# Optimization experiments

Hardware: AMD Instinct MI355X
Metric: run time of the kernel (lower is better)

Reference implementation:

```python
import jax, jax.numpy as jnp
import numpy as np

N, T, H, D = 32, 2048, 1024, 384

def setup_inputs() -> dict:
    key = jax.random.key(0)
    k1, k2, k3, k4, k5 = jax.random.split(key, 5)
    scale_h = 1.0 / np.sqrt(H)
    scale_d = 1.0 / np.sqrt(D)
    return {
        "gru_output": jax.random.normal(k1, (N, T, H), dtype=jnp.float32),
        "condition": jax.random.normal(k2, (N, D), dtype=jnp.float32),
        "W_h": jax.random.normal(k3, (H, H), dtype=jnp.float32) * scale_h,
        "W_c": jax.random.normal(k4, (D, H), dtype=jnp.float32) * scale_d,
        "bias": jnp.zeros((H,), dtype=jnp.float32),
        "v": jax.random.normal(k5, (H,), dtype=jnp.float32) * scale_h,
    }

def reference(gru_output, condition, W_h, W_c, bias, v):
    # h_proj: (N, T, H); c_proj: (N, 1, H)
    h_proj = jnp.einsum("nth,hk->ntk", gru_output, W_h)
    c_proj = jnp.einsum("nd,dk->nk", condition, W_c)[:, None, :]
    energy = jnp.tanh(h_proj + c_proj + bias)          # (N, T, H)
    scores = jnp.einsum("ntk,k->nt", energy, v)        # (N, T)
    weights = jax.nn.softmax(scores, axis=-1)          # (N, T)
    context = jnp.einsum("nth,nt->nh", gru_output, weights)  # (N, H)
    return context
```

## Files before the change

### kernel.cpp

```cpp
#include <hip/hip_runtime.h>
#include <hip/hip_bf16.h>

#define N_B 32
#define T_S 2048
#define H_D 1024
#define D_C 384
#define NT  (N_B * T_S)

typedef __attribute__((ext_vector_type(8))) short bf16x8;
typedef __attribute__((ext_vector_type(4))) float f32x4;

__device__ __forceinline__ ushort f2bf(float f) {
    union { float f; unsigned u; } x; x.f = f;
    unsigned u = x.u;
    unsigned r = (u + 0x7FFFu + ((u >> 16) & 1u)) >> 16;
    return (ushort)r;
}

__device__ __forceinline__ float bf2f(ushort u) {
    union { unsigned u; float f; } x; x.u = ((unsigned)u) << 16;
    return x.f;
}

__device__ __forceinline__ float fast_tanh(float x) {
    float e = __expf(2.0f * x);
    return 1.0f - 2.0f / (e + 1.0f);
}

__device__ __forceinline__ void gl2lds16(const void* g, void* l) {
    __builtin_amdgcn_global_load_lds(
        (const __attribute__((address_space(1))) void*)g,
        (__attribute__((address_space(3))) void*)l, 16, 0, 0);
}

__global__ __launch_bounds__(256) void convert_kernel(
    const float* __restrict__ g, ushort* __restrict__ gb)
{
    const size_t base = ((size_t)blockIdx.x * 256 + threadIdx.x) * 4;
    float4 v = *(const float4*)(g + base);
    ushort4 o;
    o.x = f2bf(v.x); o.y = f2bf(v.y); o.z = f2bf(v.z); o.w = f2bf(v.w);
    *(ushort4*)(gb + base) = o;
}

__global__ __launch_bounds__(256) void transpose_kernel(
    const float* __restrict__ W, ushort* __restrict__ Wt)
{
    __shared__ ushort tile[64 * 66];
    const int bx = blockIdx.x & 15;
    const int by = blockIdx.x >> 4;
    const int t = threadIdx.x;
    #pragma unroll
    for (int i = 0; i < 16; ++i) {
        int idx = t + i * 256;
        int r = idx >> 6, c = idx & 63;
        tile[r * 66 + c] = f2bf(W[(size_t)(by * 64 + r) * H_D + bx * 64 + c]);
    }
    __syncthreads();
    #pragma unroll
    for (int i = 0; i < 16; ++i) {
        int idx = t + i * 256;
        int r = idx >> 6, c = idx & 63;
        Wt[(size_t)(bx * 64 + r) * H_D + by * 64 + c] = tile[c * 66 + r];
    }
}

__global__ __launch_bounds__(256) void cproj_kernel(
    const float* __restrict__ cond, const float* __restrict__ Wc,
    const float* __restrict__ bias, float* __restrict__ cproj)
{
    const int idx = blockIdx.x * 256 + threadIdx.x;
    const int n = idx >> 10, k = idx & 1023;
    const int d0 = blockIdx.y * 96;
    float a0 = (blockIdx.y == 0) ? bias[k] : 0.f;
    float a1 = 0.f, a2 = 0.f, a3 = 0.f;
    const float* cp = cond + n * D_C;
    for (int d = d0; d < d0 + 96; d += 4) {
        a0 = fmaf(cp[d + 0], Wc[(size_t)(d + 0) * H_D + k], a0);
        a1 = fmaf(cp[d + 1], Wc[(size_t)(d + 1) * H_D + k], a1);
        a2 = fmaf(cp[d + 2], Wc[(size_t)(d + 2) * H_D + k], a2);
        a3 = fmaf(cp[d + 3], Wc[(size_t)(d + 3) * H_D + k], a3);
    }
    atomicAdd(&cproj[idx], (a0 + a1) + (a2 + a3));
}

__global__ __launch_bounds__(256) void gemm3_kernel(
    const ushort* __restrict__ Ab, const ushort* __restrict__ Wt,
    const float* __restrict__ cproj, const float* __restrict__ v,
    float* __restrict__ spart)
{
    __shared__ __align__(16) ushort As[128 * 64];
    __shared__ __align__(16) ushort Bs[128 * 64];
    __shared__ float red[2][2][4][16];
    const int id = blockIdx.x;
    const int mb = (id & 7) + ((id >> 6) << 3);
    const int kb = (id >> 3) & 7;
    const int m0 = mb * 128;
    const int nbatch = mb >> 4;
    const int t = threadIdx.x;
    const int lane = t & 63, wave = t >> 6;
    const int wm = wave & 1, wn = wave >> 1;
    const int q = lane >> 4, ln = lane & 15;
    const int x7 = ln & 7;

    const int srow = wave * 8 + (lane >> 3);
    const int koff = ((lane & 7) ^ (lane >> 3)) * 8;
    const ushort* ag = Ab + (size_t)(m0 + srow) * H_D + koff;
    const ushort* bg = Wt + (size_t)(kb * 128 + srow) * H_D + koff;

    f32x4 acc[4][4];
    #pragma unroll
    for (int i = 0; i < 4; ++i)
        #pragma unroll
        for (int j = 0; j < 4; ++j)
            acc[i][j] = (f32x4){0.f, 0.f, 0.f, 0.f};

    for (int h0 = 0; h0 < H_D; h0 += 64) {
        if (h0) __syncthreads();
        #pragma unroll
        for (int i = 0; i < 4; ++i) {
            gl2lds16(ag + h0 + i * 32 * H_D, As + i * 2048 + wave * 512);
            gl2lds16(bg + h0 + i * 32 * H_D, Bs + i * 2048 + wave * 512);
        }
        __syncthreads();
        #pragma unroll
        for (int kk = 0; kk < 2; ++kk) {
            bf16x8 a[4], b[4];
            #pragma unroll
            for (int i = 0; i < 4; ++i) {
                int row = wm * 64 + i * 16 + ln;
                a[i] = *(const bf16x8*)(&As[row * 64 + (((kk << 2) + q) ^ x7) * 8]);
            }
            #pragma unroll
            for (int j = 0; j < 4; ++j) {
                int row = wn * 64 + j * 16 + ln;
                b[j] = *(const bf16x8*)(&Bs[row * 64 + (((kk << 2) + q) ^ x7) * 8]);
            }
            #pragma unroll
            for (int i = 0; i < 4; ++i)
                #pragma unroll
                for (int j = 0; j < 4; ++j)
                    acc[i][j] = __builtin_amdgcn_mfma_f32_16x16x32_bf16(a[i], b[j], acc[i][j], 0, 0, 0);
        }
    }

    float cpv[4], vv[4];
    const float* cpn = cproj + nbatch * H_D;
    #pragma unroll
    for (int j = 0; j < 4; ++j) {
        int col = kb * 128 + wn * 64 + j * 16 + ln;
        cpv[j] = cpn[col];
        vv[j] = v[col];
    }
    #pragma unroll
    for (int i = 0; i < 4; ++i) {
        float s0 = 0.f, s1 = 0.f, s2 = 0.f, s3 = 0.f;
        #pragma unroll
        for (int j = 0; j < 4; ++j) {
            s0 += fast_tanh(acc[i][j][0] + cpv[j]) * vv[j];
            s1 += fast_tanh(acc[i][j][1] + cpv[j]) * vv[j];
            s2 += fast_tanh(acc[i][j][2] + cpv[j]) * vv[j];
            s3 += fast_tanh(acc[i][j][3] + cpv[j]) * vv[j];
        }
        #pragma unroll
        for (int off = 1; off < 16; off <<= 1) {
            s0 += __shfl_xor(s0, off);
            s1 += __shfl_xor(s1, off);
            s2 += __shfl_xor(s2, off);
            s3 += __shfl_xor(s3, off);
        }
        if (ln == 0) {
            red[wm][wn][i][q * 4 + 0] = s0;
            red[wm][wn][i][q * 4 + 1] = s1;
            red[wm][wn][i][q * 4 + 2] = s2;
            red[wm][wn][i][q * 4 + 3] = s3;
        }
    }
    __syncthreads();
    if (t < 128) {
        int wm2 = t >> 6, idx = t & 63;
        int i2 = idx >> 4, qr = idx & 15;
        float val = red[wm2][0][i2][qr] + red[wm2][1][i2][qr];
        spart[(size_t)kb * NT + m0 + wm2 * 64 + idx] = val;
    }
}

__global__ __launch_bounds__(1024) void softmax8_kernel(
    const float* __restrict__ spart, float* __restrict__ weights)
{
    const int n = blockIdx.x;
    const int t = threadIdx.x;
    __shared__ float red[1024];
    float s0 = 0.f, s1 = 0.f;
    #pragma unroll
    for (int kb = 0; kb < 8; ++kb) {
        s0 += spart[(size_t)kb * NT + n * T_S + t];
        s1 += spart[(size_t)kb * NT + n * T_S + 1024 + t];
    }
    red[t] = fmaxf(s0, s1); __syncthreads();
    for (int s = 512; s > 0; s >>= 1) {
        if (t < s) red[t] = fmaxf(red[t], red[t + s]);
        __syncthreads();
    }
    const float mx = red[0];
    __syncthreads();
    float e0 = __expf(s0 - mx), e1 = __expf(s1 - mx);
    red[t] = e0 + e1; __syncthreads();
    for (int s = 512; s > 0; s >>= 1) {
        if (t < s) red[t] += red[t + s];
        __syncthreads();
    }
    const float inv = 1.0f / red[0];
    weights[n * T_S + t] = e0 * inv;
    weights[n * T_S + 1024 + t] = e1 * inv;
}

__global__ __launch_bounds__(256) void context3_kernel(
    const ushort* __restrict__ Ab, const float* __restrict__ weights,
    float* __restrict__ cpart)
{
    const int tb = blockIdx.x;
    const int n  = blockIdx.y;
    const int t  = threadIdx.x;
    float a0 = 0.f, a1 = 0.f, a2 = 0.f, a3 = 0.f;
    const float* wp = weights + n * T_S + tb * 128;
    const ushort* gp = Ab + (size_t)(n * T_S + tb * 128) * H_D + t * 4;
    #pragma unroll 8
    for (int tt = 0; tt < 128; ++tt) {
        float w = wp[tt];
        ushort4 gv = *(const ushort4*)(gp + (size_t)tt * H_D);
        a0 = fmaf(w, bf2f(gv.x), a0);
        a1 = fmaf(w, bf2f(gv.y), a1);
        a2 = fmaf(w, bf2f(gv.z), a2);
        a3 = fmaf(w, bf2f(gv.w), a3);
    }
    *(float4*)(cpart + ((size_t)tb * N_B + n) * H_D + t * 4) =
        make_float4(a0, a1, a2, a3);
}

__global__ __launch_bounds__(256) void reduce_kernel(
    const float* __restrict__ cpart, float* __restrict__ out)
{
    const int idx = blockIdx.x * 256 + threadIdx.x;
    float s = 0.f;
    #pragma unroll
    for (int tb = 0; tb < 16; ++tb)
        s += cpart[(size_t)tb * (N_B * H_D) + idx];
    out[idx] = s;
}

extern "C" void kernel_launch(void* const* d_in, const int* in_sizes, int n_in,
                              void* d_out, int out_size, void* d_ws, size_t ws_size,
                              hipStream_t stream)
{
    const float* gru  = (const float*)d_in[0];
    const float* cond = (const float*)d_in[1];
    const float* W_h  = (const float*)d_in[2];
    const float* W_c  = (const float*)d_in[3];
    const float* bias = (const float*)d_in[4];
    const float* v    = (const float*)d_in[5];
    float* out = (float*)d_out;

    char* ws = (char*)d_ws;
    const size_t szAb    = (size_t)NT * H_D * 2;
    const size_t szWt    = (size_t)H_D * H_D * 2;
    const size_t szCproj = (size_t)N_B * H_D * 4;
    const size_t szSpart = (size_t)8 * NT * 4;

    ushort* Ab    = (ushort*)ws;
    ushort* Wt    = (ushort*)(ws + szAb);
    float* cproj  = (float*)(ws + szAb + szWt);
    float* spart  = (float*)(ws + szAb + szWt + szCproj);
    float* cpart  = spart;
    float* wts    = (float*)(ws + szAb + szWt + szCproj + szSpart);

    hipMemsetAsync(cproj, 0, szCproj, stream);
    convert_kernel<<<65536, 256, 0, stream>>>(gru, Ab);
    transpose_kernel<<<256, 256, 0, stream>>>(W_h, Wt);
    cproj_kernel<<<dim3(128, 4), 256, 0, stream>>>(cond, W_c, bias, cproj);
    gemm3_kernel<<<4096, 256, 0, stream>>>(Ab, Wt, cproj, v, spart);
    softmax8_kernel<<<N_B, 1024, 0, stream>>>(spart, wts);
    context3_kernel<<<dim3(16, N_B), 256, 0, stream>>>(Ab, wts, cpart);
    reduce_kernel<<<128, 256, 0, stream>>>(cpart, out);
}
```

Baseline: 560.9 us.

## Fuse fp32-to-bf16 conversion into GEMM A-tile load and drop bf16 copy

Removes the standalone conversion kernel that wrote a bf16 copy of gru_output. The GEMM now loads fp32 A tiles into registers, packs them to bf16 and writes them into swizzled LDS, while B still uses direct global-to-LDS loads. The context kernel reads fp32 gru_output directly, with more T-blocks and a matching reduction width. This removes a full write and re-read of the large intermediate. In exchange, the GEMM reads twice the bytes for A through a register-staged path, and the context pass reads fp32 instead of bf16.

```diff
diff --git a/kernel.cpp b/kernel.cpp
--- a/kernel.cpp
+++ b/kernel.cpp
@@ -17,9 +17,10 @@
     return (ushort)r;
 }
 
-__device__ __forceinline__ float bf2f(ushort u) {
-    union { unsigned u; float f; } x; x.u = ((unsigned)u) << 16;
-    return x.f;
+__device__ __forceinline__ unsigned pkbf(float a, float b) {
+    __hip_bfloat162 h = __float22bfloat162_rn(make_float2(a, b));
+    union { __hip_bfloat162 h; unsigned u; } c; c.h = h;
+    return c.u;
 }
 
 __device__ __forceinline__ float fast_tanh(float x) {
@@ -31,16 +32,6 @@
     __builtin_amdgcn_global_load_lds(
         (const __attribute__((address_space(1))) void*)g,
         (__attribute__((address_space(3))) void*)l, 16, 0, 0);
-}
-
-__global__ __launch_bounds__(256) void convert_kernel(
-    const float* __restrict__ g, ushort* __restrict__ gb)
-{
-    const size_t base = ((size_t)blockIdx.x * 256 + threadIdx.x) * 4;
-    float4 v = *(const float4*)(g + base);
-    ushort4 o;
-    o.x = f2bf(v.x); o.y = f2bf(v.y); o.z = f2bf(v.z); o.w = f2bf(v.w);
-    *(ushort4*)(gb + base) = o;
 }
 
 __global__ __launch_bounds__(256) void transpose_kernel(
@@ -84,8 +75,8 @@
     atomicAdd(&cproj[idx], (a0 + a1) + (a2 + a3));
 }
 
-__global__ __launch_bounds__(256) void gemm3_kernel(
-    const ushort* __restrict__ Ab, const ushort* __restrict__ Wt,
+__global__ __launch_bounds__(256) void gemm4_kernel(
+    const float* __restrict__ gru, const ushort* __restrict__ Wt,
     const float* __restrict__ cproj, const float* __restrict__ v,
     float* __restrict__ spart)
 {
@@ -103,9 +94,14 @@
     const int q = lane >> 4, ln = lane & 15;
     const int x7 = ln & 7;
 
+    const int arow = t >> 4;
+    const int acol = (t & 15) * 4;
+    const float* agf = gru + (size_t)(m0 + arow) * H_D + acol;
+    const int kc2 = (t & 15) >> 1;
+    const int half = (t & 1) * 4;
+
     const int srow = wave * 8 + (lane >> 3);
     const int koff = ((lane & 7) ^ (lane >> 3)) * 8;
-    const ushort* ag = Ab + (size_t)(m0 + srow) * H_D + koff;
     const ushort* bg = Wt + (size_t)(kb * 128 + srow) * H_D + koff;
 
     f32x4 acc[4][4];
@@ -116,11 +112,19 @@
             acc[i][j] = (f32x4){0.f, 0.f, 0.f, 0.f};
 
     for (int h0 = 0; h0 < H_D; h0 += 64) {
+        float4 av[8];
+        #pragma unroll
+        for (int i = 0; i < 8; ++i)
+            av[i] = *(const float4*)(agf + h0 + (size_t)i * 16 * H_D);
         if (h0) __syncthreads();
         #pragma unroll
-        for (int i = 0; i < 4; ++i) {
-            gl2lds16(ag + h0 + i * 32 * H_D, As + i * 2048 + wave * 512);
+        for (int i = 0; i < 4; ++i)
             gl2lds16(bg + h0 + i * 32 * H_D, Bs + i * 2048 + wave * 512);
+        #pragma unroll
+        for (int i = 0; i < 8; ++i) {
+            int row = i * 16 + arow;
+            uint2 p = make_uint2(pkbf(av[i].x, av[i].y), pkbf(av[i].z, av[i].w));
+            *(uint2*)(&As[row * 64 + ((kc2 ^ (row & 7)) << 3) + half]) = p;
         }
         __syncthreads();
         #pragma unroll
@@ -215,24 +219,24 @@
     weights[n * T_S + 1024 + t] = e1 * inv;
 }
 
-__global__ __launch_bounds__(256) void context3_kernel(
-    const ushort* __restrict__ Ab, const float* __restrict__ weights,
+__global__ __launch_bounds__(256) void context4_kernel(
+    const float* __restrict__ gru, const float* __restrict__ weights,
     float* __restrict__ cpart)
 {
     const int tb = blockIdx.x;
     const int n  = blockIdx.y;
     const int t  = threadIdx.x;
     float a0 = 0.f, a1 = 0.f, a2 = 0.f, a3 = 0.f;
-    const float* wp = weights + n * T_S + tb * 128;
-    const ushort* gp = Ab + (size_t)(n * T_S + tb * 128) * H_D + t * 4;
+    const float* wp = weights + n * T_S + tb * 64;
+    const float* gp = gru + (size_t)(n * T_S + tb * 64) * H_D + t * 4;
     #pragma unroll 8
-    for (int tt = 0; tt < 128; ++tt) {
+    for (int tt = 0; tt < 64; ++tt) {
         float w = wp[tt];
-        ushort4 gv = *(const ushort4*)(gp + (size_t)tt * H_D);
-        a0 = fmaf(w, bf2f(gv.x), a0);
-        a1 = fmaf(w, bf2f(gv.y), a1);
-        a2 = fmaf(w, bf2f(gv.z), a2);
-        a3 = fmaf(w, bf2f(gv.w), a3);
+        float4 gv = *(const float4*)(gp + (size_t)tt * H_D);
+        a0 = fmaf(w, gv.x, a0);
+        a1 = fmaf(w, gv.y, a1);
+        a2 = fmaf(w, gv.z, a2);
+        a3 = fmaf(w, gv.w, a3);
     }
     *(float4*)(cpart + ((size_t)tb * N_B + n) * H_D + t * 4) =
         make_float4(a0, a1, a2, a3);
@@ -244,7 +248,7 @@
     const int idx = blockIdx.x * 256 + threadIdx.x;
     float s = 0.f;
     #pragma unroll
-    for (int tb = 0; tb < 16; ++tb)
+    for (int tb = 0; tb < 32; ++tb)
         s += cpart[(size_t)tb * (N_B * H_D) + idx];
     out[idx] = s;
 }
@@ -262,24 +266,22 @@
     float* out = (float*)d_out;
 
     char* ws = (char*)d_ws;
-    const size_t szAb    = (size_t)NT * H_D * 2;
     const size_t szWt    = (size_t)H_D * H_D * 2;
     const size_t szCproj = (size_t)N_B * H_D * 4;
     const size_t szSpart = (size_t)8 * NT * 4;
-
-    ushort* Ab    = (ushort*)ws;
-    ushort* Wt    = (ushort*)(ws + szAb);
-    float* cproj  = (float*)(ws + szAb + szWt);
-    float* spart  = (float*)(ws + szAb + szWt + szCproj);
-    float* cpart  = spart;
-    float* wts    = (float*)(ws + szAb + szWt + szCproj + szSpart);
+    const size_t szWts   = (size_t)NT * 4;
+
+    ushort* Wt    = (ushort*)ws;
+    float* cproj  = (float*)(ws + szWt);
+    float* spart  = (float*)(ws + szWt + szCproj);
+    float* wts    = (float*)(ws + szWt + szCproj + szSpart);
+    float* cpart  = (float*)(ws + szWt + szCproj + szSpart + szWts);
 
     hipMemsetAsync(cproj, 0, szCproj, stream);
-    convert_kernel<<<65536, 256, 0, stream>>>(gru, Ab);
     transpose_kernel<<<256, 256, 0, stream>>>(W_h, Wt);
     cproj_kernel<<<dim3(128, 4), 256, 0, stream>>>(cond, W_c, bias, cproj);
-    gemm3_kernel<<<4096, 256, 0, stream>>>(Ab, Wt, cproj, v, spart);
+    gemm4_kernel<<<4096, 256, 0, stream>>>(gru, Wt, cproj, v, spart);
     softmax8_kernel<<<N_B, 1024, 0, stream>>>(spart, wts);
-    context3_kernel<<<dim3(16, N_B), 256, 0, stream>>>(Ab, wts, cpart);
+    context4_kernel<<<dim3(32, N_B), 256, 0, stream>>>(gru, wts, cpart);
     reduce_kernel<<<128, 256, 0, stream>>>(cpart, out);
 }
```

Result: no change. 562.6 us (+0.3%).
